# Kernel tuning notes

Measured on AMD Instinct MI355X. Metric: run time of the kernel, lower is better.

## Reference

```python
import jax, jax.numpy as jnp
import numpy as np

# ---- static config (matches init_kwargs / langevin args) ----
B, N, D = 2, 16384, 3
F_DIM = 128      # feature_net.out_channels
H_DIM = 128      # score_net hidden
N_BLOCKS = 2
K = 4            # denoise_knn
NUM_STEPS = 4
STEP_SIZE = 0.2
STEP_DECAY = 0.95

# static sliding-window neighbor indices, computed once (numpy -> constant)
_offsets = np.arange(-(K - 1) // 2, (K - 1) // 2 + 1)
NBR_IDX = np.clip(np.arange(N)[:, None] + _offsets, 0, N - 1)   # (N, K)
NBR_FLAT = NBR_IDX.reshape(-1)                                  # (N*K,)


def setup_inputs() -> dict:
    key = jax.random.key(0)
    ks = jax.random.split(key, 8)
    s = 0.05
    return {
        "pcl_noisy": jax.random.normal(ks[0], (B, N, D), jnp.float32),
        "Wf1": jax.random.normal(ks[1], (D, F_DIM), jnp.float32) * s,
        "bf1": jnp.zeros((F_DIM,), jnp.float32),
        "Wf2": jax.random.normal(ks[2], (F_DIM, F_DIM), jnp.float32) * s,
        "bf2": jnp.zeros((F_DIM,), jnp.float32),
        "W0": jax.random.normal(ks[3], (D + F_DIM, H_DIM), jnp.float32) * s,
        "b0": jnp.zeros((H_DIM,), jnp.float32),
        "Wb": jax.random.normal(ks[4], (N_BLOCKS, H_DIM, H_DIM), jnp.float32) * s,
        "bb": jnp.zeros((N_BLOCKS, H_DIM), jnp.float32),
        "Wo": jax.random.normal(ks[5], (H_DIM, D), jnp.float32) * s,
        "bo": jnp.zeros((D,), jnp.float32),
    }


def _feature_net(pcl, Wf1, bf1, Wf2, bf2):
    # pointwise MLP: (B,N,3) -> (B,N,F)
    h = jax.nn.relu(pcl @ Wf1 + bf1)
    return h @ Wf2 + bf2


def _score_net(x_cent, feat, W0, b0, Wb, bb, Wo, bo):
    # x_cent: (B,N,K,3) centered frames, feat: (B,N,F) per-seed context
    c = jnp.broadcast_to(feat[:, :, None, :], x_cent.shape[:3] + (feat.shape[-1],))
    h = jax.nn.relu(jnp.concatenate([x_cent, c], axis=-1) @ W0 + b0)  # (B,N,K,H)
    for i in range(N_BLOCKS):  # small fixed residual stack
        h = h + jax.nn.relu(h @ Wb[i] + bb[i])
    return h @ Wo + bo  # (B,N,K,3)


def reference(pcl_noisy, Wf1, bf1, Wf2, bf2, W0, b0, Wb, bb, Wo, bo):
    feat = _feature_net(pcl_noisy, Wf1, bf1, Wf2, bf2)  # (B,N,F), computed once

    def step(pcl_next, step_i):
        frames = pcl_next[:, NBR_IDX, :]                      # gather (B,N,K,3)
        centered = frames - pcl_noisy[:, :, None, :]          # center on original cloud
        grad_pred = _score_net(centered, feat, W0, b0, Wb, bb, Wo, bo)  # (B,N,K,3)
        acc = jnp.zeros_like(pcl_noisy).at[:, NBR_FLAT, :].add(
            grad_pred.reshape(pcl_noisy.shape[0], -1, D))     # scatter_add (B,N,3)
        s = STEP_SIZE * (STEP_DECAY ** step_i.astype(jnp.float32))
        return pcl_next + s * acc, None

    pcl_next, _ = jax.lax.scan(step, pcl_noisy, jnp.arange(NUM_STEPS))
    return pcl_next
```

## Files before the change

### kernel.cpp

```cpp
#include <hip/hip_runtime.h>

#define NPT    16384
#define TOTP   32768
#define FD     128
#define CHK    64
#define FTILES (TOTP/32)
#define FGRP   (FTILES/2)

typedef unsigned short u16;
typedef __attribute__((ext_vector_type(8))) short bf16x8;
typedef __attribute__((ext_vector_type(4))) float f32x4;

__device__ __forceinline__ float bf2f(u16 u) {
    union { unsigned int i; float f; } v; v.i = ((unsigned int)u) << 16; return v.f;
}
__device__ __forceinline__ u16 f2bf(float f) {
    union { float f; unsigned int i; } v; v.f = f;
    unsigned int u = v.i;
    u = u + 0x7FFFu + ((u >> 16) & 1u);
    return (u16)(u >> 16);
}
__device__ __forceinline__ int swz(int row, int colbyte) {
    return row*256 + (colbyte ^ ((row & 7) << 4));
}

__global__ __launch_bounds__(256, 2) void fproj_mfma(
    const float* __restrict__ pcl, const float* __restrict__ Wf1,
    const float* __restrict__ bf1, const float* __restrict__ Wf2,
    const float* __restrict__ bf2, const float* __restrict__ W0,
    const float* __restrict__ b0, u16* __restrict__ fproj)
{
    __shared__ __align__(16) char hA[16384];
    __shared__ __align__(16) char hB[16384];
    const int tid = threadIdx.x, wid = tid >> 6, l = tid & 63;
    const int l15 = l & 15, l4 = l >> 4;
    const int colb = wid * 32;

    bf16x8 wfA[2][4], wfB[2][4];
    #pragma unroll
    for (int ntg = 0; ntg < 2; ++ntg)
        #pragma unroll
        for (int kk = 0; kk < 4; ++kk) {
            bf16x8 fa, fb;
            #pragma unroll
            for (int e = 0; e < 8; ++e) {
                int k = kk*32 + l4*8 + e;
                int n = colb + ntg*16 + l15;
                fa[e] = (short)f2bf(Wf2[k*FD + n]);
                fb[e] = (short)f2bf(W0[(3+k)*FD + n]);
            }
            wfA[ntg][kk] = fa; wfB[ntg][kk] = fb;
        }
    float wf1c[3][2], bf1v[2], bf2v[2], b0v[2];
    #pragma unroll
    for (int ntg = 0; ntg < 2; ++ntg) {
        int col = colb + ntg*16 + l15;
        wf1c[0][ntg] = Wf1[0*FD+col];
        wf1c[1][ntg] = Wf1[1*FD+col];
        wf1c[2][ntg] = Wf1[2*FD+col];
        bf1v[ntg] = bf1[col]; bf2v[ntg] = bf2[col]; b0v[ntg] = b0[col];
    }

    for (int grp = blockIdx.x; grp < FGRP; grp += gridDim.x) {
        #pragma unroll
        for (int t = 0; t < 2; ++t) {
            char* hAt = hA + t*8192;
            const int pt0 = (grp*2 + t)*32;
            #pragma unroll
            for (int rt = 0; rt < 2; ++rt)
                #pragma unroll
                for (int reg = 0; reg < 4; ++reg) {
                    int row = rt*16 + l4*4 + reg;
                    int p = pt0 + row;
                    float px = pcl[p*3+0], py = pcl[p*3+1], pz = pcl[p*3+2];
                    #pragma unroll
                    for (int ntg = 0; ntg < 2; ++ntg) {
                        float tv = bf1v[ntg] + px*wf1c[0][ntg] + py*wf1c[1][ntg] + pz*wf1c[2][ntg];
                        tv = fmaxf(tv, 0.f);
                        int col = colb + ntg*16 + l15;
                        *(u16*)(hAt + swz(row, col*2)) = f2bf(tv);
                    }
                }
        }
        __syncthreads();
        #pragma unroll
        for (int t = 0; t < 2; ++t) {
            char* hAt = hA + t*8192;
            char* hBt = hB + t*8192;
            bf16x8 a[2][4];
            #pragma unroll
            for (int rt = 0; rt < 2; ++rt)
                #pragma unroll
                for (int kk = 0; kk < 4; ++kk)
                    a[rt][kk] = *(const bf16x8*)(hAt + swz(rt*16 + l15, kk*64 + l4*16));
            #pragma unroll
            for (int ntg = 0; ntg < 2; ++ntg) {
                f32x4 acc0 = {bf2v[ntg],bf2v[ntg],bf2v[ntg],bf2v[ntg]};
                f32x4 acc1 = acc0;
                #pragma unroll
                for (int kk = 0; kk < 4; ++kk) {
                    acc0 = __builtin_amdgcn_mfma_f32_16x16x32_bf16(a[0][kk], wfA[ntg][kk], acc0, 0,0,0);
                    acc1 = __builtin_amdgcn_mfma_f32_16x16x32_bf16(a[1][kk], wfA[ntg][kk], acc1, 0,0,0);
                }
                int col = colb + ntg*16 + l15;
                #pragma unroll
                for (int reg = 0; reg < 4; ++reg) {
                    *(u16*)(hBt + swz(l4*4+reg,    col*2)) = f2bf(acc0[reg]);
                    *(u16*)(hBt + swz(16+l4*4+reg, col*2)) = f2bf(acc1[reg]);
                }
            }
        }
        __syncthreads();
        #pragma unroll
        for (int t = 0; t < 2; ++t) {
            char* hBt = hB + t*8192;
            const int pt0 = (grp*2 + t)*32;
            bf16x8 a[2][4];
            #pragma unroll
            for (int rt = 0; rt < 2; ++rt)
                #pragma unroll
                for (int kk = 0; kk < 4; ++kk)
                    a[rt][kk] = *(const bf16x8*)(hBt + swz(rt*16 + l15, kk*64 + l4*16));
            #pragma unroll
            for (int ntg = 0; ntg < 2; ++ntg) {
                f32x4 acc0 = {b0v[ntg],b0v[ntg],b0v[ntg],b0v[ntg]};
                f32x4 acc1 = acc0;
                #pragma unroll
                for (int kk = 0; kk < 4; ++kk) {
                    acc0 = __builtin_amdgcn_mfma_f32_16x16x32_bf16(a[0][kk], wfB[ntg][kk], acc0, 0,0,0);
                    acc1 = __builtin_amdgcn_mfma_f32_16x16x32_bf16(a[1][kk], wfB[ntg][kk], acc1, 0,0,0);
                }
                int col = colb + ntg*16 + l15;
                #pragma unroll
                for (int reg = 0; reg < 4; ++reg) {
                    fproj[(size_t)(pt0 + l4*4+reg)*FD + col]      = f2bf(acc0[reg]);
                    fproj[(size_t)(pt0 + 16 + l4*4+reg)*FD + col] = f2bf(acc1[reg]);
                }
            }
        }
        __syncthreads();
    }
}

__global__ __launch_bounds__(256, 2) void fused_steps(
    const float* __restrict__ pcl, const u16* __restrict__ fproj,
    const float* __restrict__ W0, const float* __restrict__ Wb,
    const float* __restrict__ bb, const float* __restrict__ Wo,
    const float* __restrict__ bo, float* __restrict__ out)
{
    __shared__ __align__(16) u16   fpl[86*144];
    __shared__ __align__(16) float X0l[88*3];
    __shared__ __align__(16) float Xal[88*3];
    __shared__ __align__(16) float Xbl[88*3];
    __shared__ __align__(16) char  hA[8192];
    __shared__ __align__(16) char  hB[8192];
    __shared__ __align__(16) char  hC[8192];

    const int tid = threadIdx.x, wid = tid >> 6, l = tid & 63;
    const int l15 = l & 15, l4 = l >> 4;
    const int colb = wid * 32;

    const int blk = blockIdx.x;
    const int b = blk >> 8, cidx = blk & 255;
    const int A = cidx * CHK, Bp = A + CHK - 1;
    const int elo  = (A - 12 < 0) ? 0 : A - 12;
    const int ehi  = (Bp + 12 > NPT-1) ? NPT-1 : Bp + 12;
    const int esz3 = (ehi - elo + 1) * 3;
    const int fqlo = (A - 10 < 0) ? 0 : A - 10;
    const int fqhi = (Bp + 11 > NPT-1) ? NPT-1 : Bp + 11;
    const int fqc  = fqhi - fqlo + 1;
    const size_t gb = (size_t)b * NPT;

    bf16x8 wfrag[2][2][4];
    #pragma unroll
    for (int layer = 0; layer < 2; ++layer)
        #pragma unroll
        for (int ntg = 0; ntg < 2; ++ntg)
            #pragma unroll
            for (int kk = 0; kk < 4; ++kk) {
                bf16x8 f;
                #pragma unroll
                for (int e = 0; e < 8; ++e) {
                    int k = kk*32 + l4*8 + e;
                    int n = colb + ntg*16 + l15;
                    f[e] = (short)f2bf(Wb[layer*FD*FD + k*FD + n]);
                }
                wfrag[layer][ntg][kk] = f;
            }
    bf16x8 wofrag[4];
    #pragma unroll
    for (int kk = 0; kk < 4; ++kk) {
        bf16x8 f;
        #pragma unroll
        for (int e = 0; e < 8; ++e) {
            int k = kk*32 + l4*8 + e;
            f[e] = (short)(l15 < 3 ? f2bf(Wo[k*3 + l15]) : 0);
        }
        wofrag[kk] = f;
    }
    float w0c[3][2], bbv[2][2];
    #pragma unroll
    for (int ntg = 0; ntg < 2; ++ntg) {
        int col = colb + ntg*16 + l15;
        w0c[0][ntg] = W0[0*FD+col];
        w0c[1][ntg] = W0[1*FD+col];
        w0c[2][ntg] = W0[2*FD+col];
        bbv[0][ntg] = bb[col]; bbv[1][ntg] = bb[FD+col];
    }
    const float bol = (l15 < 3) ? bo[l15] : 0.f;

    for (int i = tid; i < esz3; i += 256) X0l[i] = pcl[(gb + elo)*3 + i];
    for (int i = tid; i < fqc*32; i += 256) {
        int r = i >> 5, c = i & 31;
        *(uint2*)&fpl[r*144 + c*4] = *(const uint2*)&fproj[(gb + fqlo + r)*FD + c*4];
    }
    __syncthreads();

    auto do_step = [&](const float* curl, float* nxtl, float sval, int qlo, int qhi) {
        for (int i = tid; i < esz3; i += 256) nxtl[i] = curl[i];
        __syncthreads();
        const int nt_ = (qhi - qlo + 8) >> 3;
        for (int t = 0; t < nt_; ++t) {
            const int qbase = qlo + t*8;
            float hc[2][2][4];
            #pragma unroll
            for (int rt = 0; rt < 2; ++rt) {
                int q = qbase + rt*4 + l4; if (q > qhi) q = qhi;
                int qe = (q - elo)*3;
                float nx = X0l[qe], ny = X0l[qe+1], nz = X0l[qe+2];
                float cx[4], cy[4], cz[4];
                #pragma unroll
                for (int k = 0; k < 4; ++k) {
                    int nb = q + k - 2;
                    nb = nb < 0 ? 0 : (nb > NPT-1 ? NPT-1 : nb);
                    int te = (nb - elo)*3;
                    cx[k] = curl[te]   - nx;
                    cy[k] = curl[te+1] - ny;
                    cz[k] = curl[te+2] - nz;
                }
                #pragma unroll
                for (int ntg = 0; ntg < 2; ++ntg) {
                    int col = colb + ntg*16 + l15;
                    float fp = bf2f(fpl[(q - fqlo)*144 + col]);
                    #pragma unroll
                    for (int reg = 0; reg < 4; ++reg) {
                        float u = fp + cx[reg]*w0c[0][ntg] + cy[reg]*w0c[1][ntg] + cz[reg]*w0c[2][ntg];
                        u = fmaxf(u, 0.f);
                        hc[rt][ntg][reg] = u;
                        *(u16*)(hA + swz(rt*16 + l4*4 + reg, col*2)) = f2bf(u);
                    }
                }
            }
            __syncthreads();
            {
                bf16x8 a[2][4];
                #pragma unroll
                for (int rt = 0; rt < 2; ++rt)
                    #pragma unroll
                    for (int kk = 0; kk < 4; ++kk)
                        a[rt][kk] = *(const bf16x8*)(hA + swz(rt*16 + l15, kk*64 + l4*16));
                #pragma unroll
                for (int ntg = 0; ntg < 2; ++ntg) {
                    f32x4 acc0 = {bbv[0][ntg],bbv[0][ntg],bbv[0][ntg],bbv[0][ntg]};
                    f32x4 acc1 = acc0;
                    #pragma unroll
                    for (int kk = 0; kk < 4; ++kk) {
                        acc0 = __builtin_amdgcn_mfma_f32_16x16x32_bf16(a[0][kk], wfrag[0][ntg][kk], acc0, 0,0,0);
                        acc1 = __builtin_amdgcn_mfma_f32_16x16x32_bf16(a[1][kk], wfrag[0][ntg][kk], acc1, 0,0,0);
                    }
                    int col = colb + ntg*16 + l15;
                    #pragma unroll
                    for (int reg = 0; reg < 4; ++reg) {
                        hc[0][ntg][reg] += fmaxf(acc0[reg], 0.f);
                        hc[1][ntg][reg] += fmaxf(acc1[reg], 0.f);
                        *(u16*)(hB + swz(l4*4+reg,    col*2)) = f2bf(hc[0][ntg][reg]);
                        *(u16*)(hB + swz(16+l4*4+reg, col*2)) = f2bf(hc[1][ntg][reg]);
                    }
                }
            }
            __syncthreads();
            {
                bf16x8 a[2][4];
                #pragma unroll
                for (int rt = 0; rt < 2; ++rt)
                    #pragma unroll
                    for (int kk = 0; kk < 4; ++kk)
                        a[rt][kk] = *(const bf16x8*)(hB + swz(rt*16 + l15, kk*64 + l4*16));
                #pragma unroll
                for (int ntg = 0; ntg < 2; ++ntg) {
                    f32x4 acc0 = {bbv[1][ntg],bbv[1][ntg],bbv[1][ntg],bbv[1][ntg]};
                    f32x4 acc1 = acc0;
                    #pragma unroll
                    for (int kk = 0; kk < 4; ++kk) {
                        acc0 = __builtin_amdgcn_mfma_f32_16x16x32_bf16(a[0][kk], wfrag[1][ntg][kk], acc0, 0,0,0);
                        acc1 = __builtin_amdgcn_mfma_f32_16x16x32_bf16(a[1][kk], wfrag[1][ntg][kk], acc1, 0,0,0);
                    }
                    int col = colb + ntg*16 + l15;
                    #pragma unroll
                    for (int reg = 0; reg < 4; ++reg) {
                        float h0 = hc[0][ntg][reg] + fmaxf(acc0[reg], 0.f);
                        float h1 = hc[1][ntg][reg] + fmaxf(acc1[reg], 0.f);
                        *(u16*)(hC + swz(l4*4+reg,    col*2)) = f2bf(h0);
                        *(u16*)(hC + swz(16+l4*4+reg, col*2)) = f2bf(h1);
                    }
                }
            }
            __syncthreads();
            if (wid < 2) {
                const int sub = wid;
                bf16x8 a[4];
                #pragma unroll
                for (int kk = 0; kk < 4; ++kk)
                    a[kk] = *(const bf16x8*)(hC + swz(sub*16 + l15, kk*64 + l4*16));
                f32x4 acc = {0.f,0.f,0.f,0.f};
                #pragma unroll
                for (int kk = 0; kk < 4; ++kk)
                    acc = __builtin_amdgcn_mfma_f32_16x16x32_bf16(a[kk], wofrag[kk], acc, 0,0,0);
                int q = qbase + sub*4 + l4;
                if (l15 < 3 && q <= qhi) {
                    #pragma unroll
                    for (int reg = 0; reg < 4; ++reg) {
                        int nb = q + reg - 2;
                        nb = nb < 0 ? 0 : (nb > NPT-1 ? NPT-1 : nb);
                        atomicAdd(&nxtl[(nb - elo)*3 + l15], sval*(acc[reg] + bol));
                    }
                }
            }
        }
        __syncthreads();
    };

    const int q1lo = fqlo,                          q1hi = fqhi;
    const int q2lo = (A-7  < 0) ? 0 : A-7,          q2hi = (Bp+8 > NPT-1) ? NPT-1 : Bp+8;
    const int q3lo = (A-4  < 0) ? 0 : A-4,          q3hi = (Bp+5 > NPT-1) ? NPT-1 : Bp+5;
    const int q4lo = (A-1  < 0) ? 0 : A-1,          q4hi = (Bp+2 > NPT-1) ? NPT-1 : Bp+2;

    do_step(X0l, Xal, 0.2f,      q1lo, q1hi);
    do_step(Xal, Xbl, 0.19f,     q2lo, q2hi);
    do_step(Xbl, Xal, 0.1805f,   q3lo, q3hi);
    do_step(Xal, Xbl, 0.171475f, q4lo, q4hi);

    for (int i = tid; i < CHK*3; i += 256)
        out[(gb + A)*3 + i] = Xbl[(A - elo)*3 + i];
}

extern "C" void kernel_launch(void* const* d_in, const int* in_sizes, int n_in,
                              void* d_out, int out_size, void* d_ws, size_t ws_size,
                              hipStream_t stream) {
    const float* pcl = (const float*)d_in[0];
    const float* Wf1 = (const float*)d_in[1];
    const float* bf1 = (const float*)d_in[2];
    const float* Wf2 = (const float*)d_in[3];
    const float* bf2 = (const float*)d_in[4];
    const float* W0  = (const float*)d_in[5];
    const float* b0  = (const float*)d_in[6];
    const float* Wb  = (const float*)d_in[7];
    const float* bb  = (const float*)d_in[8];
    const float* Wo  = (const float*)d_in[9];
    const float* bo  = (const float*)d_in[10];
    float* out = (float*)d_out;

    u16* fproj = (u16*)d_ws;

    fproj_mfma<<<512, 256, 0, stream>>>(pcl, Wf1, bf1, Wf2, bf2, W0, b0, fproj);
    fused_steps<<<512, 256, 0, stream>>>(pcl, fproj, W0, Wb, bb, Wo, bo, out);
}
```

Baseline: 192.8 us.

## Prepack bf16 weight fragments, halve chunk size, raise occupancy, use hardware bf16 convert

Adds a prep kernel that converts the weights once into bf16 in MFMA fragment order, so each block loads its fragments with vector loads instead of per-element strided fp32 loads and conversions. The fused step kernel now works on 32-point chunks with twice as many blocks, smaller shared buffers and a third LDS buffer folded into hA, which allows 4 blocks per CU. Software bf16 rounding is swapped for the HIP intrinsic. Smaller chunks raise the relative halo recompute and add an extra kernel launch, and the moved barrier adds a sync per step.

```diff
diff --git a/kernel.cpp b/kernel.cpp
--- a/kernel.cpp
+++ b/kernel.cpp
@@ -1,11 +1,18 @@
 #include <hip/hip_runtime.h>
+#include <hip/hip_bf16.h>
 
 #define NPT    16384
 #define TOTP   32768
 #define FD     128
-#define CHK    64
-#define FTILES (TOTP/32)
-#define FGRP   (FTILES/2)
+#define CHK    32
+#define CPB    (NPT/CHK)
+#define FGRP   ((TOTP/32)/2)
+
+#define OFF_WFA 0
+#define OFF_WFB 16384
+#define OFF_WB  32768
+#define OFF_WO  98304
+#define PREP_TOT 100352
 
 typedef unsigned short u16;
 typedef __attribute__((ext_vector_type(8))) short bf16x8;
@@ -20,15 +27,51 @@
     u = u + 0x7FFFu + ((u >> 16) & 1u);
     return (u16)(u >> 16);
 }
+__device__ __forceinline__ u16 f2bf_hw(float f) {
+    __hip_bfloat16 h = __float2bfloat16(f);
+    return *(u16*)&h;
+}
 __device__ __forceinline__ int swz(int row, int colbyte) {
     return row*256 + (colbyte ^ ((row & 7) << 4));
 }
 
+__global__ __launch_bounds__(256) void prep_weights(
+    const float* __restrict__ Wf2, const float* __restrict__ W0,
+    const float* __restrict__ Wb,  const float* __restrict__ Wo,
+    u16* __restrict__ W)
+{
+    int t = blockIdx.x*256 + threadIdx.x;
+    if (t >= PREP_TOT) return;
+    float val;
+    if (t < OFF_WB) {
+        int u = t & 16383;
+        int e = u & 7, l = (u >> 3) & 63, kk = (u >> 9) & 3;
+        int ntg = (u >> 11) & 1, wid = (u >> 12) & 3;
+        int col = wid*32 + ntg*16 + (l & 15);
+        int k   = kk*32 + (l >> 4)*8 + e;
+        val = (t < OFF_WFB) ? Wf2[k*FD + col] : W0[(3+k)*FD + col];
+    } else if (t < OFF_WO) {
+        int u = t - OFF_WB;
+        int e = u & 7, l = (u >> 3) & 63, kk = (u >> 9) & 3;
+        int ntg = (u >> 11) & 1, layer = (u >> 12) & 1, wid = (u >> 13) & 3;
+        int col = wid*32 + ntg*16 + (l & 15);
+        int k   = kk*32 + (l >> 4)*8 + e;
+        val = Wb[layer*FD*FD + k*FD + col];
+    } else {
+        int u = t - OFF_WO;
+        int e = u & 7, l = (u >> 3) & 63, kk = (u >> 9) & 3;
+        int l15 = l & 15;
+        int k   = kk*32 + (l >> 4)*8 + e;
+        val = (l15 < 3) ? Wo[k*3 + l15] : 0.f;
+    }
+    W[t] = f2bf(val);
+}
+
 __global__ __launch_bounds__(256, 2) void fproj_mfma(
     const float* __restrict__ pcl, const float* __restrict__ Wf1,
-    const float* __restrict__ bf1, const float* __restrict__ Wf2,
-    const float* __restrict__ bf2, const float* __restrict__ W0,
-    const float* __restrict__ b0, u16* __restrict__ fproj)
+    const float* __restrict__ bf1, const float* __restrict__ bf2,
+    const float* __restrict__ b0,  const u16* __restrict__ Wprep,
+    u16* __restrict__ fproj)
 {
     __shared__ __align__(16) char hA[16384];
     __shared__ __align__(16) char hB[16384];
@@ -37,20 +80,18 @@
     const int colb = wid * 32;
 
     bf16x8 wfA[2][4], wfB[2][4];
-    #pragma unroll
-    for (int ntg = 0; ntg < 2; ++ntg)
-        #pragma unroll
-        for (int kk = 0; kk < 4; ++kk) {
-            bf16x8 fa, fb;
-            #pragma unroll
-            for (int e = 0; e < 8; ++e) {
-                int k = kk*32 + l4*8 + e;
-                int n = colb + ntg*16 + l15;
-                fa[e] = (short)f2bf(Wf2[k*FD + n]);
-                fb[e] = (short)f2bf(W0[(3+k)*FD + n]);
-            }
-            wfA[ntg][kk] = fa; wfB[ntg][kk] = fb;
-        }
+    {
+        const bf16x8* fa = (const bf16x8*)(Wprep + OFF_WFA);
+        const bf16x8* fb = (const bf16x8*)(Wprep + OFF_WFB);
+        #pragma unroll
+        for (int ntg = 0; ntg < 2; ++ntg)
+            #pragma unroll
+            for (int kk = 0; kk < 4; ++kk) {
+                int fi = ((wid*2 + ntg)*4 + kk)*64 + l;
+                wfA[ntg][kk] = fa[fi];
+                wfB[ntg][kk] = fb[fi];
+            }
+    }
     float wf1c[3][2], bf1v[2], bf2v[2], b0v[2];
     #pragma unroll
     for (int ntg = 0; ntg < 2; ++ntg) {
@@ -78,7 +119,7 @@
                         float tv = bf1v[ntg] + px*wf1c[0][ntg] + py*wf1c[1][ntg] + pz*wf1c[2][ntg];
                         tv = fmaxf(tv, 0.f);
                         int col = colb + ntg*16 + l15;
-                        *(u16*)(hAt + swz(row, col*2)) = f2bf(tv);
+                        *(u16*)(hAt + swz(row, col*2)) = f2bf_hw(tv);
                     }
                 }
         }
@@ -105,8 +146,8 @@
                 int col = colb + ntg*16 + l15;
                 #pragma unroll
                 for (int reg = 0; reg < 4; ++reg) {
-                    *(u16*)(hBt + swz(l4*4+reg,    col*2)) = f2bf(acc0[reg]);
-                    *(u16*)(hBt + swz(16+l4*4+reg, col*2)) = f2bf(acc1[reg]);
+                    *(u16*)(hBt + swz(l4*4+reg,    col*2)) = f2bf_hw(acc0[reg]);
+                    *(u16*)(hBt + swz(16+l4*4+reg, col*2)) = f2bf_hw(acc1[reg]);
                 }
             }
         }
@@ -133,8 +174,8 @@
                 int col = colb + ntg*16 + l15;
                 #pragma unroll
                 for (int reg = 0; reg < 4; ++reg) {
-                    fproj[(size_t)(pt0 + l4*4+reg)*FD + col]      = f2bf(acc0[reg]);
-                    fproj[(size_t)(pt0 + 16 + l4*4+reg)*FD + col] = f2bf(acc1[reg]);
+                    fproj[(size_t)(pt0 + l4*4+reg)*FD + col]      = f2bf_hw(acc0[reg]);
+                    fproj[(size_t)(pt0 + 16 + l4*4+reg)*FD + col] = f2bf_hw(acc1[reg]);
                 }
             }
         }
@@ -142,26 +183,25 @@
     }
 }
 
-__global__ __launch_bounds__(256, 2) void fused_steps(
+__global__ __launch_bounds__(256, 4) void fused_steps(
     const float* __restrict__ pcl, const u16* __restrict__ fproj,
-    const float* __restrict__ W0, const float* __restrict__ Wb,
-    const float* __restrict__ bb, const float* __restrict__ Wo,
-    const float* __restrict__ bo, float* __restrict__ out)
+    const float* __restrict__ W0, const u16* __restrict__ Wprep,
+    const float* __restrict__ bb, const float* __restrict__ bo,
+    float* __restrict__ out)
 {
-    __shared__ __align__(16) u16   fpl[86*144];
-    __shared__ __align__(16) float X0l[88*3];
-    __shared__ __align__(16) float Xal[88*3];
-    __shared__ __align__(16) float Xbl[88*3];
+    __shared__ __align__(16) u16   fpl[56*144];
+    __shared__ __align__(16) float X0l[60*3];
+    __shared__ __align__(16) float Xal[60*3];
+    __shared__ __align__(16) float Xbl[60*3];
     __shared__ __align__(16) char  hA[8192];
     __shared__ __align__(16) char  hB[8192];
-    __shared__ __align__(16) char  hC[8192];
 
     const int tid = threadIdx.x, wid = tid >> 6, l = tid & 63;
     const int l15 = l & 15, l4 = l >> 4;
     const int colb = wid * 32;
 
     const int blk = blockIdx.x;
-    const int b = blk >> 8, cidx = blk & 255;
+    const int b = blk >> 9, cidx = blk & (CPB - 1);
     const int A = cidx * CHK, Bp = A + CHK - 1;
     const int elo  = (A - 12 < 0) ? 0 : A - 12;
     const int ehi  = (Bp + 12 > NPT-1) ? NPT-1 : Bp + 12;
@@ -171,32 +211,19 @@
     const int fqc  = fqhi - fqlo + 1;
     const size_t gb = (size_t)b * NPT;
 
-    bf16x8 wfrag[2][2][4];
-    #pragma unroll
-    for (int layer = 0; layer < 2; ++layer)
-        #pragma unroll
-        for (int ntg = 0; ntg < 2; ++ntg)
-            #pragma unroll
-            for (int kk = 0; kk < 4; ++kk) {
-                bf16x8 f;
-                #pragma unroll
-                for (int e = 0; e < 8; ++e) {
-                    int k = kk*32 + l4*8 + e;
-                    int n = colb + ntg*16 + l15;
-                    f[e] = (short)f2bf(Wb[layer*FD*FD + k*FD + n]);
-                }
-                wfrag[layer][ntg][kk] = f;
-            }
-    bf16x8 wofrag[4];
-    #pragma unroll
-    for (int kk = 0; kk < 4; ++kk) {
-        bf16x8 f;
-        #pragma unroll
-        for (int e = 0; e < 8; ++e) {
-            int k = kk*32 + l4*8 + e;
-            f[e] = (short)(l15 < 3 ? f2bf(Wo[k*3 + l15]) : 0);
-        }
-        wofrag[kk] = f;
+    bf16x8 wfrag[2][2][4], wofrag[4];
+    {
+        const bf16x8* wb = (const bf16x8*)(Wprep + OFF_WB);
+        #pragma unroll
+        for (int layer = 0; layer < 2; ++layer)
+            #pragma unroll
+            for (int ntg = 0; ntg < 2; ++ntg)
+                #pragma unroll
+                for (int kk = 0; kk < 4; ++kk)
+                    wfrag[layer][ntg][kk] = wb[(((wid*2+layer)*2+ntg)*4+kk)*64 + l];
+        const bf16x8* wo = (const bf16x8*)(Wprep + OFF_WO);
+        #pragma unroll
+        for (int kk = 0; kk < 4; ++kk) wofrag[kk] = wo[kk*64 + l];
     }
     float w0c[3][2], bbv[2][2];
     #pragma unroll
@@ -247,7 +274,7 @@
                         float u = fp + cx[reg]*w0c[0][ntg] + cy[reg]*w0c[1][ntg] + cz[reg]*w0c[2][ntg];
                         u = fmaxf(u, 0.f);
                         hc[rt][ntg][reg] = u;
-                        *(u16*)(hA + swz(rt*16 + l4*4 + reg, col*2)) = f2bf(u);
+                        *(u16*)(hA + swz(rt*16 + l4*4 + reg, col*2)) = f2bf_hw(u);
                     }
                 }
             }
@@ -273,8 +300,8 @@
                     for (int reg = 0; reg < 4; ++reg) {
                         hc[0][ntg][reg] += fmaxf(acc0[reg], 0.f);
                         hc[1][ntg][reg] += fmaxf(acc1[reg], 0.f);
-                        *(u16*)(hB + swz(l4*4+reg,    col*2)) = f2bf(hc[0][ntg][reg]);
-                        *(u16*)(hB + swz(16+l4*4+reg, col*2)) = f2bf(hc[1][ntg][reg]);
+                        *(u16*)(hB + swz(l4*4+reg,    col*2)) = f2bf_hw(hc[0][ntg][reg]);
+                        *(u16*)(hB + swz(16+l4*4+reg, col*2)) = f2bf_hw(hc[1][ntg][reg]);
                     }
                 }
             }
@@ -300,8 +327,8 @@
                     for (int reg = 0; reg < 4; ++reg) {
                         float h0 = hc[0][ntg][reg] + fmaxf(acc0[reg], 0.f);
                         float h1 = hc[1][ntg][reg] + fmaxf(acc1[reg], 0.f);
-                        *(u16*)(hC + swz(l4*4+reg,    col*2)) = f2bf(h0);
-                        *(u16*)(hC + swz(16+l4*4+reg, col*2)) = f2bf(h1);
+                        *(u16*)(hA + swz(l4*4+reg,    col*2)) = f2bf_hw(h0);
+                        *(u16*)(hA + swz(16+l4*4+reg, col*2)) = f2bf_hw(h1);
                     }
                 }
             }
@@ -311,7 +338,7 @@
                 bf16x8 a[4];
                 #pragma unroll
                 for (int kk = 0; kk < 4; ++kk)
-                    a[kk] = *(const bf16x8*)(hC + swz(sub*16 + l15, kk*64 + l4*16));
+                    a[kk] = *(const bf16x8*)(hA + swz(sub*16 + l15, kk*64 + l4*16));
                 f32x4 acc = {0.f,0.f,0.f,0.f};
                 #pragma unroll
                 for (int kk = 0; kk < 4; ++kk)
@@ -326,14 +353,14 @@
                     }
                 }
             }
+            __syncthreads();
         }
-        __syncthreads();
     };
 
-    const int q1lo = fqlo,                          q1hi = fqhi;
-    const int q2lo = (A-7  < 0) ? 0 : A-7,          q2hi = (Bp+8 > NPT-1) ? NPT-1 : Bp+8;
-    const int q3lo = (A-4  < 0) ? 0 : A-4,          q3hi = (Bp+5 > NPT-1) ? NPT-1 : Bp+5;
-    const int q4lo = (A-1  < 0) ? 0 : A-1,          q4hi = (Bp+2 > NPT-1) ? NPT-1 : Bp+2;
+    const int q1lo = fqlo,                 q1hi = fqhi;
+    const int q2lo = (A-7 < 0) ? 0 : A-7,  q2hi = (Bp+8 > NPT-1) ? NPT-1 : Bp+8;
+    const int q3lo = (A-4 < 0) ? 0 : A-4,  q3hi = (Bp+5 > NPT-1) ? NPT-1 : Bp+5;
+    const int q4lo = (A-1 < 0) ? 0 : A-1,  q4hi = (Bp+2 > NPT-1) ? NPT-1 : Bp+2;
 
     do_step(X0l, Xal, 0.2f,      q1lo, q1hi);
     do_step(Xal, Xbl, 0.19f,     q2lo, q2hi);
@@ -360,8 +387,10 @@
     const float* bo  = (const float*)d_in[10];
     float* out = (float*)d_out;
 
-    u16* fproj = (u16*)d_ws;
-
-    fproj_mfma<<<512, 256, 0, stream>>>(pcl, Wf1, bf1, Wf2, bf2, W0, b0, fproj);
-    fused_steps<<<512, 256, 0, stream>>>(pcl, fproj, W0, Wb, bb, Wo, bo, out);
-}
+    u16* Wprep = (u16*)d_ws;
+    u16* fproj = (u16*)((char*)d_ws + PREP_TOT*2);
+
+    prep_weights<<<(PREP_TOT+255)/256, 256, 0, stream>>>(Wf2, W0, Wb, Wo, Wprep);
+    fproj_mfma<<<512, 256, 0, stream>>>(pcl, Wf1, bf1, bf2, b0, Wprep, fproj);
+    fused_steps<<<2*CPB, 256, 0, stream>>>(pcl, fproj, W0, Wprep, bb, bo, out);
+}
```

After: 380.8 us. +97.5%, slower.
